# Kernel tuning notes

Hardware: AMD Instinct MI355X
Metric: run time of the kernel (lower is better)

Reference implementation:

```python
import jax, jax.numpy as jnp
import numpy as np

WS = 11        # gaussian window size
SIGMA = 1.5    # gaussian sigma
L = 10.0       # val_range
SSIM_C1 = (0.01 * L) ** 2
SSIM_C2 = (0.03 * L) ** 2


def _window():
    g = jnp.exp(-((jnp.arange(WS) - WS // 2) ** 2) / (2.0 * SIGMA ** 2))
    g = g / g.sum()
    return jnp.outer(g, g).astype(jnp.float32)  # [11,11], sums to 1


def _blur(z, win):
    # depthwise 11x11 gaussian blur with VALID padding; z: [..., H, W]
    lead = z.shape[:-2]
    zf = z.reshape((-1, 1) + z.shape[-2:])
    out = jax.lax.conv_general_dilated(zf, win[None, None], (1, 1), 'VALID')
    return out.reshape(lead + out.shape[-2:])


def setup_inputs() -> dict:
    key = jax.random.key(0)
    ks = jax.random.split(key, 7)
    B, C, Fc, H, W = 8, 64, 3, 192, 192
    return {
        'x': jax.random.normal(ks[0], (B, C, H, W), jnp.float32),
        'x_feature': jax.random.normal(ks[1], (B, Fc, H, W), jnp.float32),
        'spatial_w': jax.random.normal(ks[2], (1, Fc, 3, 1), jnp.float32) * 0.1,
        'W1': jax.random.normal(ks[3], (C, C), jnp.float32) * 0.05,
        'b1': jnp.zeros((C,), jnp.float32),
        'W2': jax.random.normal(ks[4], (C, C), jnp.float32) * 0.05,
        'b2': jnp.zeros((C,), jnp.float32),
    }


def reference(x, x_feature, spatial_w, W1, b1, W2, b2):
    win = _window()
    # per-channel gaussian moments (computed once, reused across all pairs)
    mu_x = _blur(x, win)                         # [B,C,h,w]
    mu_f = _blur(x_feature, win)                 # [B,F,h,w]
    sig_x = _blur(x * x, win) - mu_x ** 2        # variance of x channels
    sig_f = _blur(x_feature * x_feature, win) - mu_f ** 2
    # all pairwise cross-covariances in one batched blur
    prod = x_feature[:, :, None] * x[:, None]    # [B,F,C,H,W]
    sig_fx = _blur(prod, win) - mu_f[:, :, None] * mu_x[:, None]
    v1 = 2.0 * sig_fx + SSIM_C2
    v2 = sig_f[:, :, None] + sig_x[:, None] + SSIM_C2
    num = (2.0 * mu_f[:, :, None] * mu_x[:, None] + SSIM_C1) * v1
    den = (mu_f[:, :, None] ** 2 + mu_x[:, None] ** 2 + SSIM_C1) * v2
    ssim_info = (num / den).mean(axis=(-2, -1))  # [B,F,C]
    # spatial gate: Conv2d(3,1,(3,1),padding=(1,0)) over [B,F,C,1]
    si4 = ssim_info[..., None]                   # [B,F,C,1]
    h = jax.lax.conv_general_dilated(si4, spatial_w, (1, 1), ((1, 1), (0, 0)))
    h = jax.nn.relu(h).reshape(x.shape[0], -1)   # [B,C]
    h = jax.nn.relu(h @ W1.T + b1) @ W2.T + b2
    return jax.nn.sigmoid(h), ssim_info
```

## Files before the change

kernel.cpp:

```cpp
#include <hip/hip_runtime.h>
#include <math.h>

#define HW 192
#define OW 182
#define NPIX (OW*OW)
#define NTILE 8
#define SSIM_C1 0.01f
#define SSIM_C2 0.09f

#define Gk0 0.0010283835f
#define Gk1 0.0075987615f
#define Gk2 0.0360007700f
#define Gk3 0.1093608000f
#define Gk4 0.2130055400f
#define Gk5 0.2660117000f

typedef float v2f __attribute__((ext_vector_type(2)));

__device__ __forceinline__ v2f vfma(float w, v2f a, v2f b) {
    return __builtin_elementwise_fma((v2f){w, w}, a, b);
}
__device__ __forceinline__ v2f vfma2(v2f w, v2f a, v2f b) {
    return __builtin_elementwise_fma(w, a, b);
}

__device__ __forceinline__ void dgauss(float g[11]) {
    float s = 0.f;
#pragma unroll
    for (int i = 0; i < 11; ++i) {
        float d = (float)(i - 5);
        g[i] = expf(-(d * d) / 4.5f);
        s += g[i];
    }
    float inv = 1.f / s;
#pragma unroll
    for (int i = 0; i < 11; ++i) g[i] *= inv;
}

__global__ __launch_bounds__(256) void muf_kernel(const float* __restrict__ xf,
                                                  float* __restrict__ muf,
                                                  float* __restrict__ sigc2f) {
    const int tile = blockIdx.x % 14;
    const int img  = blockIdx.x / 14;
    const int r0   = tile * 13;

    __shared__ float raw[23][192];
    __shared__ float hb[2][23][184];

    float g[11]; dgauss(g);
    const int t = threadIdx.x;
    const float* src = xf + (size_t)img * HW * HW;

    for (int i = t; i < 23 * 192; i += 256) {
        int rr = i / 192, col = i - rr * 192;
        raw[rr][col] = src[(r0 + rr) * HW + col];
    }
    __syncthreads();

    for (int i = t; i < 23 * OW; i += 256) {
        int rr = i / OW, co = i - rr * OW;
        float a0 = 0.f, a1 = 0.f;
#pragma unroll
        for (int k = 0; k < 11; ++k) {
            float v = raw[rr][co + k];
            float w = g[k];
            a0 += w * v;
            a1 += w * v * v;
        }
        hb[0][rr][co] = a0;
        hb[1][rr][co] = a1;
    }
    __syncthreads();

    for (int i = t; i < 13 * OW; i += 256) {
        int rr = i / OW, co = i - rr * OW;
        float m = 0.f, s2 = 0.f;
#pragma unroll
        for (int k = 0; k < 11; ++k) {
            float w = g[k];
            m  += w * hb[0][rr + k][co];
            s2 += w * hb[1][rr + k][co];
        }
        size_t o = (size_t)img * NPIX + (size_t)(r0 + rr) * OW + co;
        muf[o]    = m;
        sigc2f[o] = s2 - m * m + SSIM_C2;
    }
}

__global__ __launch_bounds__(192, 3) void ssim_kernel(const float* __restrict__ x,
                                                      const float* __restrict__ xf,
                                                      const float* __restrict__ muf,
                                                      const float* __restrict__ sigc2f,
                                                      float* __restrict__ part) {
    const float G[11] = {Gk0,Gk1,Gk2,Gk3,Gk4,Gk5,Gk4,Gk3,Gk2,Gk1,Gk0};
    const v2f WA[6] = {{G[0],0.f},{G[2],G[1]},{G[4],G[3]},{G[6],G[5]},{G[8],G[7]},{G[10],G[9]}};
    const v2f WB[6] = {{G[1],G[0]},{G[3],G[2]},{G[5],G[4]},{G[7],G[6]},{G[9],G[8]},{0.f,G[10]}};

    const int blk  = blockIdx.x;
    const int c    = blk & 63;
    const int tile = (blk >> 6) & 7;
    const int b    = blk >> 9;

    const int out0  = (tile * 182) >> 3;
    const int out1  = ((tile + 1) * 182) >> 3;
    const int n_out = out1 - out0;

    const int t    = threadIdx.x;
    const int half = (t >= 96) ? 1 : 0;
    const int u    = half ? (t - 96) : t;
    const int cu   = 2 * u;
    const bool act = (u <= 90);

    const float* xp  = x  + ((size_t)(b * 64 + c)) * HW * HW + (size_t)out0 * HW + t;
    const float* fp0 = xf + ((size_t)(b * 3 + 0)) * HW * HW + (size_t)out0 * HW + t;
    const float* fp1 = fp0 + HW * HW;
    const float* fp2 = fp1 + HW * HW;

    const float* mp = muf    + (size_t)(b * 3) * NPIX + (size_t)(out0 + half) * OW + cu;
    const float* cp = sigc2f + (size_t)(b * 3) * NPIX + (size_t)(out0 + half) * OW + cu;

    __shared__ float eb[8][5][192];
    __shared__ float red[3][3];

    v2f P01[10], P23[10];
    float P4[10];
#pragma unroll
    for (int j = 0; j < 10; ++j) { P01[j] = (v2f){0.f,0.f}; P23[j] = (v2f){0.f,0.f}; P4[j] = 0.f; }

    v2f A0 = {0.f,0.f}, A1 = {0.f,0.f}, A2 = {0.f,0.f};

    v2f eE01, eE23; float eE4;

    auto vstep = [&](float xv, float a0, float a1, float a2, bool emit) {
        v2f v01 = {xv, xv * xv};
        v2f v23 = {xv * a0, xv * a1};
        float v4 = xv * a2;
        if (emit) {
            eE01 = vfma(G[10], v01, P01[0]);
            eE23 = vfma(G[10], v23, P23[0]);
            eE4  = fmaf(G[10], v4, P4[0]);
        }
#pragma unroll
        for (int j = 0; j < 9; ++j) {
            P01[j] = vfma(G[9 - j], v01, P01[j + 1]);
            P23[j] = vfma(G[9 - j], v23, P23[j + 1]);
            P4[j]  = fmaf(G[9 - j], v4, P4[j + 1]);
        }
        P01[9] = G[0] * v01;
        P23[9] = G[0] * v23;
        P4[9]  = G[0] * v4;
    };

    auto ssim2 = [&](const v2f mux, const v2f mux2, const v2f sigc,
                     const v2f mf, const v2f cc, const v2f h, v2f& A) {
        v2f t1  = mf * mux;
        v2f sfx = h - t1;
        v2f v1s = vfma(2.f, sfx, (v2f){SSIM_C2, SSIM_C2});
        v2f n1  = vfma(2.f, t1, (v2f){SSIM_C1, SSIM_C1});
        v2f num = n1 * v1s;
        v2f qd  = vfma2(mf, mf, (v2f){SSIM_C1, SSIM_C1});
        v2f den = (qd + mux2) * (cc + sigc);
        v2f inv = {__builtin_amdgcn_rcpf(den.x), __builtin_amdgcn_rcpf(den.y)};
        A = vfma2(num, inv, A);
    };

    auto store_e = [&](int slot) {
        eb[slot][0][t] = eE01.x; eb[slot][1][t] = eE01.y;
        eb[slot][2][t] = eE23.x; eb[slot][3][t] = eE23.y;
        eb[slot][4][t] = eE4;
    };

    auto do_row = [&](int slot, int mrow) {
        v2f mf0 = *(const v2f*)(mp + mrow);
        v2f mf1 = *(const v2f*)(mp + mrow + NPIX);
        v2f mf2 = *(const v2f*)(mp + mrow + 2 * NPIX);
        v2f cc0 = *(const v2f*)(cp + mrow);
        v2f cc1 = *(const v2f*)(cp + mrow + NPIX);
        v2f cc2 = *(const v2f*)(cp + mrow + 2 * NPIX);
        v2f hacc[5];
#pragma unroll
        for (int f = 0; f < 5; ++f) {
            const float* ep = &eb[slot][f][cu];
            v2f a = {0.f, 0.f};
#pragma unroll
            for (int m = 0; m < 6; ++m) {
                v2f rd = *(const v2f*)(ep + 2 * m);
                a = vfma2(WA[m], __builtin_shufflevector(rd, rd, 0, 0), a);
                a = vfma2(WB[m], __builtin_shufflevector(rd, rd, 1, 1), a);
            }
            hacc[f] = a;
        }
        const v2f mux  = hacc[0];
        const v2f mux2 = mux * mux;
        const v2f sigc = hacc[1] - mux2;
        ssim2(mux, mux2, sigc, mf0, cc0, hacc[2], A0);
        ssim2(mux, mux2, sigc, mf1, cc1, hacc[3], A1);
        ssim2(mux, mux2, sigc, mf2, cc2, hacc[4], A2);
    };

#pragma unroll 1
    for (int r = 0; r < 10; r += 2) {
        float xA0 = xp[0],  a00 = fp0[0],  a10 = fp1[0],  a20 = fp2[0];
        float xB0 = xp[HW], b00 = fp0[HW], b10 = fp1[HW], b20 = fp2[HW];
        xp += 2 * HW; fp0 += 2 * HW; fp1 += 2 * HW; fp2 += 2 * HW;
        vstep(xA0, a00, a10, a20, false);
        vstep(xB0, b00, b10, b20, false);
    }

    const int ngrp = (n_out + 3) >> 2;

    float cx[4], c0[4], c1[4], c2[4];
#pragma unroll
    for (int q = 0; q < 4; ++q) {
        cx[q] = xp[q * HW]; c0[q] = fp0[q * HW];
        c1[q] = fp1[q * HW]; c2[q] = fp2[q * HW];
    }
    xp += 4 * HW; fp0 += 4 * HW; fp1 += 4 * HW; fp2 += 4 * HW;

#pragma unroll 1
    for (int p = 0; p < ngrp; ++p) {
        float nx[4], n0[4], n1[4], n2[4];
        {
            const int rb = 4 * p + 4;
#pragma unroll
            for (int q = 0; q < 4; ++q) {
                const int off = (((rb + q) < n_out) ? q : (n_out - 1 - rb)) * HW;
                nx[q] = xp[off]; n0[q] = fp0[off];
                n1[q] = fp1[off]; n2[q] = fp2[off];
            }
            xp += 4 * HW; fp0 += 4 * HW; fp1 += 4 * HW; fp2 += 4 * HW;
        }

#pragma unroll
        for (int q = 0; q < 4; ++q) {
            const int e = 4 * p + q;
            if (e < n_out) {
                vstep(cx[q], c0[q], c1[q], c2[q], true);
                store_e(e & 7);
            }
        }
        __syncthreads();

#pragma unroll
        for (int q = 0; q < 4; ++q) {
            cx[q] = nx[q]; c0[q] = n0[q]; c1[q] = n1[q]; c2[q] = n2[q];
        }

        if (act) do_row((4 * p + half) & 7, 0);

        if (act && (4 * p + 2 + half) < n_out) do_row((4 * p + 2 + half) & 7, 2 * OW);

        mp += 4 * OW; cp += 4 * OW;
    }

    float acc0 = A0.x + A0.y;
    float acc1 = A1.x + A1.y;
    float acc2 = A2.x + A2.y;
#pragma unroll
    for (int off = 32; off > 0; off >>= 1) {
        acc0 += __shfl_down(acc0, off);
        acc1 += __shfl_down(acc1, off);
        acc2 += __shfl_down(acc2, off);
    }
    const int wid = t >> 6, lane = t & 63;
    if (lane == 0) { red[0][wid] = acc0; red[1][wid] = acc1; red[2][wid] = acc2; }
    __syncthreads();
    if (t == 0) {
        const size_t o = (size_t)tile * 1536 + (size_t)b * 192;
        part[o +   0 + c] = red[0][0] + red[0][1] + red[0][2];
        part[o +  64 + c] = red[1][0] + red[1][1] + red[1][2];
        part[o + 128 + c] = red[2][0] + red[2][1] + red[2][2];
    }
}

__global__ __launch_bounds__(64) void gate_kernel(const float* __restrict__ part,
                                                  const float* __restrict__ sw,
                                                  const float* __restrict__ W1,
                                                  const float* __restrict__ b1,
                                                  const float* __restrict__ W2,
                                                  const float* __restrict__ b2,
                                                  float* __restrict__ out,
                                                  float* __restrict__ out_ssim) {
    const int b = blockIdx.x;
    const int c = threadIdx.x;

    __shared__ float s[3][64];
    __shared__ float h0[64];
    __shared__ float h1[64];

    const float inv = 1.f / (float)NPIX;
#pragma unroll
    for (int f = 0; f < 3; ++f) {
        const int i = b * 192 + f * 64 + c;
        float v = 0.f;
#pragma unroll
        for (int k = 0; k < NTILE; ++k) v += part[i + k * 1536];
        v *= inv;
        s[f][c] = v;
        out_ssim[i] = v;
    }
    __syncthreads();

    float a = 0.f;
#pragma unroll
    for (int f = 0; f < 3; ++f)
#pragma unroll
        for (int i = 0; i < 3; ++i) {
            int cc = c - 1 + i;
            if (cc >= 0 && cc < 64) a += sw[f * 3 + i] * s[f][cc];
        }
    h0[c] = fmaxf(a, 0.f);
    __syncthreads();

    float a1 = b1[c];
    for (int j = 0; j < 64; ++j) a1 += W1[c * 64 + j] * h0[j];
    h1[c] = fmaxf(a1, 0.f);
    __syncthreads();

    float a2 = b2[c];
    for (int j = 0; j < 64; ++j) a2 += W2[c * 64 + j] * h1[j];
    out[b * 64 + c] = 1.f / (1.f + expf(-a2));
}

extern "C" void kernel_launch(void* const* d_in, const int* in_sizes, int n_in,
                              void* d_out, int out_size, void* d_ws, size_t ws_size,
                              hipStream_t stream) {
    const float* x  = (const float*)d_in[0];
    const float* xf = (const float*)d_in[1];
    const float* sw = (const float*)d_in[2];
    const float* W1 = (const float*)d_in[3];
    const float* b1 = (const float*)d_in[4];
    const float* W2 = (const float*)d_in[5];
    const float* b2 = (const float*)d_in[6];
    float* out = (float*)d_out;

    float* muf  = (float*)d_ws;
    float* sigf = muf + 24 * NPIX;
    float* part = sigf + 24 * NPIX;

    muf_kernel <<<24 * 14,        256, 0, stream>>>(xf, muf, sigf);
    ssim_kernel<<<8 * 64 * NTILE, 192, 0, stream>>>(x, xf, muf, sigf, part);
    gate_kernel<<<8,               64, 0, stream>>>(part, sw, W1, b1, W2, b2, out, out + 512);
}
```

Baseline: 112.0 us.

## Remap horizontal pass to four output columns per thread with 128-bit LDS reads

The horizontal blur and SSIM stage now has each thread handle four adjacent output columns of one row, using 48 threads per row over four rows, instead of two columns across two rows per half-block. Each thread reads its 16-float shared window with vector loads and reuses those values for both column pairs. This cuts LDS read traffic and instruction count per output. It also hoists the first-pair mu/sigma global loads ahead of the vertical pass to hide their latency. In exchange it raises register pressure, pads the shared buffer, and drops the guard that skipped vertical steps past n_out.

```diff
diff --git a/kernel.cpp b/kernel.cpp
--- a/kernel.cpp
+++ b/kernel.cpp
@@ -16,6 +16,7 @@
 #define Gk5 0.2660117000f
 
 typedef float v2f __attribute__((ext_vector_type(2)));
+typedef float v4f __attribute__((ext_vector_type(4)));
 
 __device__ __forceinline__ v2f vfma(float w, v2f a, v2f b) {
     return __builtin_elementwise_fma((v2f){w, w}, a, b);
@@ -93,8 +94,11 @@
                                                       const float* __restrict__ sigc2f,
                                                       float* __restrict__ part) {
     const float G[11] = {Gk0,Gk1,Gk2,Gk3,Gk4,Gk5,Gk4,Gk3,Gk2,Gk1,Gk0};
-    const v2f WA[6] = {{G[0],0.f},{G[2],G[1]},{G[4],G[3]},{G[6],G[5]},{G[8],G[7]},{G[10],G[9]}};
-    const v2f WB[6] = {{G[1],G[0]},{G[3],G[2]},{G[5],G[4]},{G[7],G[6]},{G[9],G[8]},{0.f,G[10]}};
+    v2f T[12];
+    T[0] = (v2f){G[0], 0.f};
+#pragma unroll
+    for (int i = 1; i <= 10; ++i) T[i] = (v2f){G[i], G[i - 1]};
+    T[11] = (v2f){0.f, G[10]};
 
     const int blk  = blockIdx.x;
     const int c    = blk & 63;
@@ -105,21 +109,22 @@
     const int out1  = ((tile + 1) * 182) >> 3;
     const int n_out = out1 - out0;
 
-    const int t    = threadIdx.x;
-    const int half = (t >= 96) ? 1 : 0;
-    const int u    = half ? (t - 96) : t;
-    const int cu   = 2 * u;
-    const bool act = (u <= 90);
+    const int t  = threadIdx.x;
+    const int r  = t / 48;
+    const int q  = t - 48 * r;
+    const int c0 = 4 * q;
+    const bool act  = (q < 46);
+    const bool p2ok = (c0 + 2 < OW);
 
     const float* xp  = x  + ((size_t)(b * 64 + c)) * HW * HW + (size_t)out0 * HW + t;
     const float* fp0 = xf + ((size_t)(b * 3 + 0)) * HW * HW + (size_t)out0 * HW + t;
     const float* fp1 = fp0 + HW * HW;
     const float* fp2 = fp1 + HW * HW;
 
-    const float* mp = muf    + (size_t)(b * 3) * NPIX + (size_t)(out0 + half) * OW + cu;
-    const float* cp = sigc2f + (size_t)(b * 3) * NPIX + (size_t)(out0 + half) * OW + cu;
-
-    __shared__ float eb[8][5][192];
+    const float* mp = muf    + (size_t)(b * 3) * NPIX + (size_t)(out0 + r) * OW + c0;
+    const float* cp = sigc2f + (size_t)(b * 3) * NPIX + (size_t)(out0 + r) * OW + c0;
+
+    __shared__ __align__(16) float eb[8][5][208];
     __shared__ float red[3][3];
 
     v2f P01[10], P23[10];
@@ -170,36 +175,8 @@
         eb[slot][4][t] = eE4;
     };
 
-    auto do_row = [&](int slot, int mrow) {
-        v2f mf0 = *(const v2f*)(mp + mrow);
-        v2f mf1 = *(const v2f*)(mp + mrow + NPIX);
-        v2f mf2 = *(const v2f*)(mp + mrow + 2 * NPIX);
-        v2f cc0 = *(const v2f*)(cp + mrow);
-        v2f cc1 = *(const v2f*)(cp + mrow + NPIX);
-        v2f cc2 = *(const v2f*)(cp + mrow + 2 * NPIX);
-        v2f hacc[5];
-#pragma unroll
-        for (int f = 0; f < 5; ++f) {
-            const float* ep = &eb[slot][f][cu];
-            v2f a = {0.f, 0.f};
-#pragma unroll
-            for (int m = 0; m < 6; ++m) {
-                v2f rd = *(const v2f*)(ep + 2 * m);
-                a = vfma2(WA[m], __builtin_shufflevector(rd, rd, 0, 0), a);
-                a = vfma2(WB[m], __builtin_shufflevector(rd, rd, 1, 1), a);
-            }
-            hacc[f] = a;
-        }
-        const v2f mux  = hacc[0];
-        const v2f mux2 = mux * mux;
-        const v2f sigc = hacc[1] - mux2;
-        ssim2(mux, mux2, sigc, mf0, cc0, hacc[2], A0);
-        ssim2(mux, mux2, sigc, mf1, cc1, hacc[3], A1);
-        ssim2(mux, mux2, sigc, mf2, cc2, hacc[4], A2);
-    };
-
 #pragma unroll 1
-    for (int r = 0; r < 10; r += 2) {
+    for (int rr = 0; rr < 10; rr += 2) {
         float xA0 = xp[0],  a00 = fp0[0],  a10 = fp1[0],  a20 = fp2[0];
         float xB0 = xp[HW], b00 = fp0[HW], b10 = fp1[HW], b20 = fp2[HW];
         xp += 2 * HW; fp0 += 2 * HW; fp1 += 2 * HW; fp2 += 2 * HW;
@@ -209,46 +186,100 @@
 
     const int ngrp = (n_out + 3) >> 2;
 
-    float cx[4], c0[4], c1[4], c2[4];
-#pragma unroll
-    for (int q = 0; q < 4; ++q) {
-        cx[q] = xp[q * HW]; c0[q] = fp0[q * HW];
-        c1[q] = fp1[q * HW]; c2[q] = fp2[q * HW];
+    float cx[4], cf0[4], cf1[4], cf2[4];
+#pragma unroll
+    for (int j = 0; j < 4; ++j) {
+        cx[j]  = xp[j * HW];  cf0[j] = fp0[j * HW];
+        cf1[j] = fp1[j * HW]; cf2[j] = fp2[j * HW];
     }
     xp += 4 * HW; fp0 += 4 * HW; fp1 += 4 * HW; fp2 += 4 * HW;
 
 #pragma unroll 1
     for (int p = 0; p < ngrp; ++p) {
-        float nx[4], n0[4], n1[4], n2[4];
+        float nx[4], nf0[4], nf1[4], nf2[4];
         {
             const int rb = 4 * p + 4;
 #pragma unroll
-            for (int q = 0; q < 4; ++q) {
-                const int off = (((rb + q) < n_out) ? q : (n_out - 1 - rb)) * HW;
-                nx[q] = xp[off]; n0[q] = fp0[off];
-                n1[q] = fp1[off]; n2[q] = fp2[off];
+            for (int j = 0; j < 4; ++j) {
+                const int off = (((rb + j) < n_out) ? j : (n_out - 1 - rb)) * HW;
+                nx[j]  = xp[off];  nf0[j] = fp0[off];
+                nf1[j] = fp1[off]; nf2[j] = fp2[off];
             }
             xp += 4 * HW; fp0 += 4 * HW; fp1 += 4 * HW; fp2 += 4 * HW;
         }
 
-#pragma unroll
-        for (int q = 0; q < 4; ++q) {
-            const int e = 4 * p + q;
-            if (e < n_out) {
-                vstep(cx[q], c0[q], c1[q], c2[q], true);
-                store_e(e & 7);
-            }
+        const bool row_ok = act && (4 * p + r < n_out);
+
+        v2f mfa0, mfa1, mfa2, cca0, cca1, cca2;
+        if (row_ok) {
+            mfa0 = *(const v2f*)(mp);
+            mfa1 = *(const v2f*)(mp + NPIX);
+            mfa2 = *(const v2f*)(mp + 2 * NPIX);
+            cca0 = *(const v2f*)(cp);
+            cca1 = *(const v2f*)(cp + NPIX);
+            cca2 = *(const v2f*)(cp + 2 * NPIX);
+        }
+
+#pragma unroll
+        for (int j = 0; j < 4; ++j) {
+            vstep(cx[j], cf0[j], cf1[j], cf2[j], true);
+            store_e((4 * p + j) & 7);
         }
         __syncthreads();
 
 #pragma unroll
-        for (int q = 0; q < 4; ++q) {
-            cx[q] = nx[q]; c0[q] = n0[q]; c1[q] = n1[q]; c2[q] = n2[q];
-        }
-
-        if (act) do_row((4 * p + half) & 7, 0);
-
-        if (act && (4 * p + 2 + half) < n_out) do_row((4 * p + 2 + half) & 7, 2 * OW);
+        for (int j = 0; j < 4; ++j) {
+            cx[j] = nx[j]; cf0[j] = nf0[j]; cf1[j] = nf1[j]; cf2[j] = nf2[j];
+        }
+
+        if (row_ok) {
+            const int slot = (4 * p + r) & 7;
+            v2f h01[5], h23[5];
+#pragma unroll
+            for (int f = 0; f < 5; ++f) {
+                const float* ep = &eb[slot][f][c0];
+                v4f w0 = *(const v4f*)(ep);
+                v4f w1 = *(const v4f*)(ep + 4);
+                v4f w2 = *(const v4f*)(ep + 8);
+                v4f w3 = *(const v4f*)(ep + 12);
+                const float w[16] = {w0.x,w0.y,w0.z,w0.w, w1.x,w1.y,w1.z,w1.w,
+                                     w2.x,w2.y,w2.z,w2.w, w3.x,w3.y,w3.z,w3.w};
+                v2f o01 = {0.f,0.f}, o23 = {0.f,0.f};
+#pragma unroll
+                for (int i = 0; i < 12; ++i) {
+                    o01 = vfma2(T[i], (v2f){w[i],     w[i]},     o01);
+                    o23 = vfma2(T[i], (v2f){w[i + 2], w[i + 2]}, o23);
+                }
+                h01[f] = o01; h23[f] = o23;
+            }
+
+            v2f mfb0, mfb1, mfb2, ccb0, ccb1, ccb2;
+            if (p2ok) {
+                mfb0 = *(const v2f*)(mp + 2);
+                mfb1 = *(const v2f*)(mp + NPIX + 2);
+                mfb2 = *(const v2f*)(mp + 2 * NPIX + 2);
+                ccb0 = *(const v2f*)(cp + 2);
+                ccb1 = *(const v2f*)(cp + NPIX + 2);
+                ccb2 = *(const v2f*)(cp + 2 * NPIX + 2);
+            }
+
+            {
+                const v2f mux  = h01[0];
+                const v2f mux2 = mux * mux;
+                const v2f sigc = h01[1] - mux2;
+                ssim2(mux, mux2, sigc, mfa0, cca0, h01[2], A0);
+                ssim2(mux, mux2, sigc, mfa1, cca1, h01[3], A1);
+                ssim2(mux, mux2, sigc, mfa2, cca2, h01[4], A2);
+            }
+            if (p2ok) {
+                const v2f mux  = h23[0];
+                const v2f mux2 = mux * mux;
+                const v2f sigc = h23[1] - mux2;
+                ssim2(mux, mux2, sigc, mfb0, ccb0, h23[2], A0);
+                ssim2(mux, mux2, sigc, mfb1, ccb1, h23[3], A1);
+                ssim2(mux, mux2, sigc, mfb2, ccb2, h23[4], A2);
+            }
+        }
 
         mp += 4 * OW; cp += 4 * OW;
     }
```

New measurement: 318.8 us. 185% more time.
